# Performance work log

Measured on AMD Instinct MI355X. Metric: run time of the kernel, lower is better.

## Reference

```python
import jax, jax.numpy as jnp
import numpy as np

EMBED_DIM = 1024
N_HEADS = 16
HEAD_SIZE = EMBED_DIM // N_HEADS
SCALE = HEAD_SIZE ** -0.5


def setup_inputs() -> dict:
    key = jax.random.key(0)
    ks = jax.random.split(key, 11)
    B, Tq, Tk, C = 4, 1024, 1024, EMBED_DIM
    std = 0.02
    return {
        "q": jax.random.normal(ks[0], (B, Tq, C), jnp.float32),
        "k": jax.random.normal(ks[1], (B, Tk, C), jnp.float32),
        "v": jax.random.normal(ks[2], (B, Tk, C), jnp.float32),
        "Wq": jax.random.normal(ks[3], (C, C), jnp.float32) * std,
        "bq": jnp.zeros((C,), jnp.float32),
        "Wk": jax.random.normal(ks[4], (C, C), jnp.float32) * std,
        "bk": jnp.zeros((C,), jnp.float32),
        "Wv": jax.random.normal(ks[5], (C, C), jnp.float32) * std,
        "bv": jnp.zeros((C,), jnp.float32),
        "Wo": jax.random.normal(ks[6], (C, C), jnp.float32) * std,
        "bo": jnp.zeros((C,), jnp.float32),
    }


def reference(q, k, v, Wq, bq, Wk, bk, Wv, bv, Wo, bo):
    b, t, c = q.shape
    # linear projections (torch Linear: x @ W.T + b)
    qp = q @ Wq.T + bq            # [b, tq, c]
    kp = k @ Wk.T + bk            # [b, tk, c]
    vp = v @ Wv.T + bv            # [b, tk, c]
    # split heads: [b, h, t, d]
    qh = qp.reshape(b, t, N_HEADS, HEAD_SIZE).transpose(0, 2, 1, 3)
    kh = kp.reshape(b, kp.shape[1], N_HEADS, HEAD_SIZE).transpose(0, 2, 1, 3)
    vh = vp.reshape(b, vp.shape[1], N_HEADS, HEAD_SIZE).transpose(0, 2, 1, 3)
    # scaled dot-product attention
    scores = jnp.einsum('bhqd,bhkd->bhqk', qh, kh) * SCALE
    weights = jax.nn.softmax(scores, axis=-1)
    attn = jnp.einsum('bhqk,bhkd->bhqd', weights, vh)
    attn = attn.transpose(0, 2, 1, 3).reshape(b, t, c)
    out = attn @ Wo.T + bo
    return out
```

## Files before the change

kernel.cpp:

```cpp
#include <hip/hip_runtime.h>
#include <stdint.h>

typedef unsigned short u16;
typedef unsigned int   u32;
typedef __bf16 bf16;
typedef bf16  bf16x8 __attribute__((ext_vector_type(8)));
typedef float f32x4  __attribute__((ext_vector_type(4)));

#define AS1 __attribute__((address_space(1)))
#define AS3 __attribute__((address_space(3)))


__device__ __forceinline__ u16 f2bf(float f) {
  u32 u = __float_as_uint(f);
  return (u16)((u + 0x7fffu + ((u >> 16) & 1u)) >> 16);
}

__device__ __forceinline__ void gload_lds16(const void* src, void* dst) {
  __builtin_amdgcn_global_load_lds((const AS1 void*)src, (AS3 void*)dst, 16, 0, 0);
}

__device__ __forceinline__ bf16x8 fragL(const char* lds, int row, int kbyte) {
  return *(const bf16x8*)(lds + row * 128 + kbyte);
}


__global__ __launch_bounds__(256) void cvt_all(
    const float* q, const float* k, const float* v,
    const float* wq, const float* wk, const float* wv, const float* wo,
    u16* qb, u16* kb, u16* vb,
    u16* wqb, u16* wkb, u16* wvb, u16* wob)
{
  const float* src; u16* dst; int n4;
  switch (blockIdx.y) {
    case 0: src = q;  dst = qb;  n4 = 1048576; break;
    case 1: src = k;  dst = kb;  n4 = 1048576; break;
    case 2: src = v;  dst = vb;  n4 = 1048576; break;
    case 3: src = wq; dst = wqb; n4 = 262144;  break;
    case 4: src = wk; dst = wkb; n4 = 262144;  break;
    case 5: src = wv; dst = wvb; n4 = 262144;  break;
    default: src = wo; dst = wob; n4 = 262144; break;
  }
  int stride = gridDim.x * blockDim.x;
  for (int i = blockIdx.x * blockDim.x + threadIdx.x; i < n4; i += stride) {
    float4 f = ((const float4*)src)[i];
    ushort4 o;
    o.x = f2bf(f.x); o.y = f2bf(f.y); o.z = f2bf(f.z); o.w = f2bf(f.w);
    ((ushort4*)dst)[i] = o;
  }
}


__device__ __forceinline__ void stageL(const u16* gtile, char* lds, int tid)
{
  int w = tid >> 6, lane = tid & 63;
  int rr = lane >> 3;
  int cb = (lane & 7) << 4;
  #pragma unroll
  for (int i = 0; i < 4; ++i) {
    int c = i * 4 + w;
    gload_lds16((const char*)(gtile + (c * 8 + rr) * 1024) + cb, lds + c * 1024);
  }
}

__device__ __forceinline__ void gemm_core(const u16* A, const u16* W,
                                          f32x4 acc[4][4], int bi, int bj,
                                          int tid, char* As, char* Bs)
{
  int lane = tid & 63;
  int wr = (tid >> 7) & 1, wc = (tid >> 6) & 1;
  for (int kt = 0; kt < 16; ++kt) {
    stageL(A + bi * 128 * 1024 + kt * 64, As, tid);
    stageL(W + bj * 128 * 1024 + kt * 64, Bs, tid);
    __syncthreads();
    #pragma unroll
    for (int ks = 0; ks < 2; ++ks) {
      int kb = ks * 64 + ((lane >> 4) << 4);
      bf16x8 af[4], bfr[4];
      #pragma unroll
      for (int m = 0; m < 4; ++m) af[m]  = fragL(As, wr * 64 + m * 16 + (lane & 15), kb);
      #pragma unroll
      for (int n = 0; n < 4; ++n) bfr[n] = fragL(Bs, wc * 64 + n * 16 + (lane & 15), kb);
      #pragma unroll
      for (int m = 0; m < 4; ++m)
        #pragma unroll
        for (int n = 0; n < 4; ++n)
          acc[m][n] = __builtin_amdgcn_mfma_f32_16x16x32_bf16(af[m], bfr[n], acc[m][n], 0, 0, 0);
    }
    __syncthreads();
  }
}


__global__ __launch_bounds__(256, 2) void proj_gemm(
    const u16* qb, const u16* kb, const u16* vb,
    const u16* wqb, const u16* wkb, const u16* wvb,
    const float* bq, const float* bk, const float* bv,
    u16* qh, u16* kh, u16* vt)
{
  __shared__ alignas(16) char As[16384];
  __shared__ alignas(16) char Bs[16384];
  int tid = threadIdx.x;
  int bi = blockIdx.x & 31, bj = blockIdx.x >> 5;
  int z = blockIdx.z;
  const u16* A = (z == 0) ? qb : (z == 1) ? kb : vb;
  const u16* W = (z == 0) ? wqb : (z == 1) ? wkb : wvb;
  const float* bias = (z == 0) ? bq : (z == 1) ? bk : bv;
  u16* dst = (z == 0) ? qh : (z == 1) ? kh : vt;

  f32x4 acc[4][4] = {};
  gemm_core(A, W, acc, bi, bj, tid, As, Bs);

  int lane = tid & 63, wr = (tid >> 7) & 1, wc = (tid >> 6) & 1;
  int rbase = bi * 128 + wr * 64 + ((lane >> 4) << 2);
  int cbase = bj * 128 + wc * 64;
  #pragma unroll
  for (int n = 0; n < 4; ++n) {
    int col = cbase + n * 16 + (lane & 15);
    float bsv = bias[col];
    int h = col >> 6, d = col & 63;
    #pragma unroll
    for (int m = 0; m < 4; ++m) {
      #pragma unroll
      for (int r = 0; r < 4; ++r) {
        int R = rbase + m * 16 + r;
        int b = R >> 10, t = R & 1023;
        u16 val = f2bf(acc[m][n][r] + bsv);
        if (z < 2) dst[(((b * 16 + h) * 1024 + t) << 6) + d] = val;
        else       dst[(((b * 16 + h) * 64 + d) << 10) + t] = val;
      }
    }
  }
}


__global__ __launch_bounds__(256, 2) void out_gemm(
    const u16* attn, const u16* wob, const float* bo, float* out)
{
  __shared__ alignas(16) char As[16384];
  __shared__ alignas(16) char Bs[16384];
  int tid = threadIdx.x;
  int bi = blockIdx.x & 31, bj = blockIdx.x >> 5;

  f32x4 acc[4][4] = {};
  gemm_core(attn, wob, acc, bi, bj, tid, As, Bs);

  int lane = tid & 63, wr = (tid >> 7) & 1, wc = (tid >> 6) & 1;
  int rbase = bi * 128 + wr * 64 + ((lane >> 4) << 2);
  int cbase = bj * 128 + wc * 64;
  #pragma unroll
  for (int n = 0; n < 4; ++n) {
    int col = cbase + n * 16 + (lane & 15);
    float bsv = bo[col];
    #pragma unroll
    for (int m = 0; m < 4; ++m) {
      #pragma unroll
      for (int r = 0; r < 4; ++r) {
        int R = rbase + m * 16 + r;
        out[R * 1024 + col] = acc[m][n][r] + bsv;
      }
    }
  }
}


__global__ __launch_bounds__(256, 2) void attn_fwd(
    const u16* qh, const u16* kh, const u16* vt, u16* attnb)
{
  __shared__ alignas(16) u16 Ks[64 * 72];
  __shared__ alignas(16) u16 Vs[64 * 72];
  __shared__ alignas(16) u16 Pl[4][16 * 72];

  int tid = threadIdx.x, lane = tid & 63, w = tid >> 6;
  int g = lane >> 4;
  int q0 = blockIdx.x << 6;
  int bh = blockIdx.y;
  const u16* qbase = qh + bh * 65536;
  const u16* kbase = kh + bh * 65536;
  const u16* vbase = vt + bh * 65536;

  bf16x8 qf[2];
  {
    int qrow = q0 + w * 16 + (lane & 15);
    const u16* p = qbase + qrow * 64 + (g << 3);
    qf[0] = *(const bf16x8*)p;
    qf[1] = *(const bf16x8*)(p + 32);
  }

  f32x4 ot[4] = {};
  float m_r = -3.0e38f, l_r = 0.f;

  int sr = tid >> 2;
  int sj = (tid & 3) << 4;
  u16* pw = Pl[w];
  int prow = (lane & 15) * 72;

  for (int kv0 = 0; kv0 < 1024; kv0 += 64) {
    {
      const u16* ksrc = kbase + (kv0 + sr) * 64 + sj;
      const u16* vsrc = vbase + sr * 1024 + kv0 + sj;
      *(bf16x8*)(Ks + sr * 72 + sj)     = *(const bf16x8*)ksrc;
      *(bf16x8*)(Ks + sr * 72 + sj + 8) = *(const bf16x8*)(ksrc + 8);
      *(bf16x8*)(Vs + sr * 72 + sj)     = *(const bf16x8*)vsrc;
      *(bf16x8*)(Vs + sr * 72 + sj + 8) = *(const bf16x8*)(vsrc + 8);
    }
    __syncthreads();

    f32x4 sc[4] = {};
    #pragma unroll
    for (int ks = 0; ks < 2; ++ks) {
      #pragma unroll
      for (int m = 0; m < 4; ++m) {
        bf16x8 kf = *(const bf16x8*)(Ks + (m * 16 + (lane & 15)) * 72 + ks * 32 + g * 8);
        sc[m] = __builtin_amdgcn_mfma_f32_16x16x32_bf16(kf, qf[ks], sc[m], 0, 0, 0);
      }
    }

    float sv[4][4];
    float vmax = -3.0e38f;
    #pragma unroll
    for (int m = 0; m < 4; ++m)
      #pragma unroll
      for (int r = 0; r < 4; ++r) {
        sv[m][r] = sc[m][r] * 0.125f;
        vmax = fmaxf(vmax, sv[m][r]);
      }
    vmax = fmaxf(vmax, __shfl_xor(vmax, 16, 64));
    vmax = fmaxf(vmax, __shfl_xor(vmax, 32, 64));
    float mnew = fmaxf(m_r, vmax);
    float fac = __expf(m_r - mnew);
    float psum = 0.f;
    u32 pp[4][2];
    #pragma unroll
    for (int m = 0; m < 4; ++m) {
      float p0 = __expf(sv[m][0] - mnew);
      float p1 = __expf(sv[m][1] - mnew);
      float p2 = __expf(sv[m][2] - mnew);
      float p3 = __expf(sv[m][3] - mnew);
      psum += (p0 + p1) + (p2 + p3);
      pp[m][0] = (u32)f2bf(p0) | ((u32)f2bf(p1) << 16);
      pp[m][1] = (u32)f2bf(p2) | ((u32)f2bf(p3) << 16);
    }
    psum += __shfl_xor(psum, 16, 64);
    psum += __shfl_xor(psum, 32, 64);
    l_r = l_r * fac + psum;
    m_r = mnew;
    #pragma unroll
    for (int dm = 0; dm < 4; ++dm) ot[dm] *= fac;

    #pragma unroll
    for (int m = 0; m < 4; ++m) {
      u32* d = (u32*)(pw + prow + m * 16 + (g << 2));
      d[0] = pp[m][0];
      d[1] = pp[m][1];
    }

    #pragma unroll
    for (int ks = 0; ks < 2; ++ks) {
      bf16x8 pf = *(const bf16x8*)(pw + prow + ks * 32 + g * 8);
      #pragma unroll
      for (int dm = 0; dm < 4; ++dm) {
        bf16x8 vf = *(const bf16x8*)(Vs + (dm * 16 + (lane & 15)) * 72 + ks * 32 + g * 8);
        ot[dm] = __builtin_amdgcn_mfma_f32_16x16x32_bf16(vf, pf, ot[dm], 0, 0, 0);
      }
    }
    __syncthreads();
  }

  float inv = 1.0f / l_r;
  int b = bh >> 4, h = bh & 15;
  int tok = (b << 10) + q0 + w * 16 + (lane & 15);
  u16* obase = attnb + tok * 1024 + h * 64;
  #pragma unroll
  for (int dm = 0; dm < 4; ++dm) {
    int d0 = dm * 16 + (g << 2);
    u32 lo = (u32)f2bf(ot[dm][0] * inv) | ((u32)f2bf(ot[dm][1] * inv) << 16);
    u32 hi = (u32)f2bf(ot[dm][2] * inv) | ((u32)f2bf(ot[dm][3] * inv) << 16);
    u32* d = (u32*)(obase + d0);
    d[0] = lo; d[1] = hi;
  }
}


extern "C" void kernel_launch(void* const* d_in, const int* in_sizes, int n_in,
                              void* d_out, int out_size, void* d_ws, size_t ws_size,
                              hipStream_t stream)
{
  const float* q  = (const float*)d_in[0];
  const float* k  = (const float*)d_in[1];
  const float* v  = (const float*)d_in[2];
  const float* Wq = (const float*)d_in[3];
  const float* bq = (const float*)d_in[4];
  const float* Wk = (const float*)d_in[5];
  const float* bk = (const float*)d_in[6];
  const float* Wv = (const float*)d_in[7];
  const float* bv = (const float*)d_in[8];
  const float* Wo = (const float*)d_in[9];
  const float* bo = (const float*)d_in[10];
  float* out = (float*)d_out;

  u16* ws  = (u16*)d_ws;
  u16* qb  = ws;
  u16* kb  = qb  + (4u << 20);
  u16* vb  = kb  + (4u << 20);
  u16* wqb = vb  + (4u << 20);
  u16* wkb = wqb + (1u << 20);
  u16* wvb = wkb + (1u << 20);
  u16* wob = wvb + (1u << 20);
  u16* qhb = wob + (1u << 20);
  u16* khb = qhb + (4u << 20);
  u16* vtb = khb + (4u << 20);
  u16* atb = vtb + (4u << 20);

  cvt_all<<<dim3(1024, 7, 1), 256, 0, stream>>>(q, k, v, Wq, Wk, Wv, Wo,
                                                qb, kb, vb, wqb, wkb, wvb, wob);
  proj_gemm<<<dim3(256, 1, 3), 256, 0, stream>>>(qb, kb, vb, wqb, wkb, wvb,
                                                 bq, bk, bv, qhb, khb, vtb);
  attn_fwd<<<dim3(16, 64, 1), 256, 0, stream>>>(qhb, khb, vtb, atb);
  out_gemm<<<dim3(256, 1, 1), 256, 0, stream>>>(atb, wob, bo, out);
}
```

Measured before the change: 224.7 us.

## Load GEMM fragments directly to registers, prefetch KV, lazy softmax rescale, native bf16 cvt

The projection and output GEMMs drop LDS staging and barriers, and each wave loads its A and W MFMA fragments straight from global memory into registers. Without shared reuse, every wave re-reads its tiles from global or cache. The attention kernel prefetches the next K/V tile into registers while the current one is computed, folds the 0.125 scale into an fmaf, and skips the online-softmax rescale unless the running max grows past a threshold. Manual bf16 rounding is replaced by native bf16 conversions.

New measurement: 285.6 us. +27.1%, slower.

```diff
diff --git a/kernel.cpp b/kernel.cpp
--- a/kernel.cpp
+++ b/kernel.cpp
@@ -4,24 +4,21 @@
 typedef unsigned short u16;
 typedef unsigned int   u32;
 typedef __bf16 bf16;
+typedef bf16  bf16x2 __attribute__((ext_vector_type(2)));
 typedef bf16  bf16x8 __attribute__((ext_vector_type(8)));
 typedef float f32x4  __attribute__((ext_vector_type(4)));
 
-#define AS1 __attribute__((address_space(1)))
-#define AS3 __attribute__((address_space(3)))
-
-
-__device__ __forceinline__ u16 f2bf(float f) {
-  u32 u = __float_as_uint(f);
-  return (u16)((u + 0x7fffu + ((u >> 16) & 1u)) >> 16);
-}
-
-__device__ __forceinline__ void gload_lds16(const void* src, void* dst) {
-  __builtin_amdgcn_global_load_lds((const AS1 void*)src, (AS3 void*)dst, 16, 0, 0);
-}
-
-__device__ __forceinline__ bf16x8 fragL(const char* lds, int row, int kbyte) {
-  return *(const bf16x8*)(lds + row * 128 + kbyte);
+
+__device__ __forceinline__ u32 pk2(float lo, float hi) {
+  bf16x2 t;
+  t[0] = (bf16)lo;
+  t[1] = (bf16)hi;
+  return __builtin_bit_cast(u32, t);
+}
+
+__device__ __forceinline__ u16 b1(float f) {
+  bf16 t = (bf16)f;
+  return __builtin_bit_cast(u16, t);
 }
 
 
@@ -44,63 +41,48 @@
   int stride = gridDim.x * blockDim.x;
   for (int i = blockIdx.x * blockDim.x + threadIdx.x; i < n4; i += stride) {
     float4 f = ((const float4*)src)[i];
-    ushort4 o;
-    o.x = f2bf(f.x); o.y = f2bf(f.y); o.z = f2bf(f.z); o.w = f2bf(f.w);
-    ((ushort4*)dst)[i] = o;
-  }
-}
-
-
-__device__ __forceinline__ void stageL(const u16* gtile, char* lds, int tid)
-{
-  int w = tid >> 6, lane = tid & 63;
-  int rr = lane >> 3;
-  int cb = (lane & 7) << 4;
-  #pragma unroll
-  for (int i = 0; i < 4; ++i) {
-    int c = i * 4 + w;
-    gload_lds16((const char*)(gtile + (c * 8 + rr) * 1024) + cb, lds + c * 1024);
-  }
-}
-
-__device__ __forceinline__ void gemm_core(const u16* A, const u16* W,
-                                          f32x4 acc[4][4], int bi, int bj,
-                                          int tid, char* As, char* Bs)
-{
-  int lane = tid & 63;
-  int wr = (tid >> 7) & 1, wc = (tid >> 6) & 1;
+    uint2 o;
+    o.x = pk2(f.x, f.y);
+    o.y = pk2(f.z, f.w);
+    ((uint2*)dst)[i] = o;
+  }
+}
+
+
+__device__ __forceinline__ void gemm_core_reg(
+    const u16* Abase, const u16* Wbase, f32x4 acc[4][4])
+{
   for (int kt = 0; kt < 16; ++kt) {
-    stageL(A + bi * 128 * 1024 + kt * 64, As, tid);
-    stageL(W + bj * 128 * 1024 + kt * 64, Bs, tid);
-    __syncthreads();
-    #pragma unroll
-    for (int ks = 0; ks < 2; ++ks) {
-      int kb = ks * 64 + ((lane >> 4) << 4);
-      bf16x8 af[4], bfr[4];
-      #pragma unroll
-      for (int m = 0; m < 4; ++m) af[m]  = fragL(As, wr * 64 + m * 16 + (lane & 15), kb);
-      #pragma unroll
-      for (int n = 0; n < 4; ++n) bfr[n] = fragL(Bs, wc * 64 + n * 16 + (lane & 15), kb);
+    int ko = kt * 64;
+    bf16x8 af[4][2], bw[4][2];
+    #pragma unroll
+    for (int m = 0; m < 4; ++m) {
+      #pragma unroll
+      for (int ks = 0; ks < 2; ++ks) {
+        af[m][ks] = *(const bf16x8*)(Abase + m * 16384 + ko + ks * 32);
+        bw[m][ks] = *(const bf16x8*)(Wbase + m * 16384 + ko + ks * 32);
+      }
+    }
+    #pragma unroll
+    for (int ks = 0; ks < 2; ++ks)
       #pragma unroll
       for (int m = 0; m < 4; ++m)
         #pragma unroll
         for (int n = 0; n < 4; ++n)
-          acc[m][n] = __builtin_amdgcn_mfma_f32_16x16x32_bf16(af[m], bfr[n], acc[m][n], 0, 0, 0);
-    }
-    __syncthreads();
-  }
-}
-
-
-__global__ __launch_bounds__(256, 2) void proj_gemm(
+          acc[m][n] = __builtin_amdgcn_mfma_f32_16x16x32_bf16(
+              af[m][ks], bw[n][ks], acc[m][n], 0, 0, 0);
+  }
+}
+
+
+__global__ __launch_bounds__(256) void proj_gemm(
     const u16* qb, const u16* kb, const u16* vb,
     const u16* wqb, const u16* wkb, const u16* wvb,
     const float* bq, const float* bk, const float* bv,
     u16* qh, u16* kh, u16* vt)
 {
-  __shared__ alignas(16) char As[16384];
-  __shared__ alignas(16) char Bs[16384];
-  int tid = threadIdx.x;
+  int tid = threadIdx.x, lane = tid & 63;
+  int g = lane >> 4, r16 = lane & 15;
   int bi = blockIdx.x & 31, bj = blockIdx.x >> 5;
   int z = blockIdx.z;
   const u16* A = (z == 0) ? qb : (z == 1) ? kb : vb;
@@ -108,15 +90,18 @@
   const float* bias = (z == 0) ? bq : (z == 1) ? bk : bv;
   u16* dst = (z == 0) ? qh : (z == 1) ? kh : vt;
 
+  int wr = (tid >> 7) & 1, wc = (tid >> 6) & 1;
+  const u16* Abase = A + (bi * 128 + wr * 64 + r16) * 1024 + g * 8;
+  const u16* Wbase = W + (bj * 128 + wc * 64 + r16) * 1024 + g * 8;
+
   f32x4 acc[4][4] = {};
-  gemm_core(A, W, acc, bi, bj, tid, As, Bs);
-
-  int lane = tid & 63, wr = (tid >> 7) & 1, wc = (tid >> 6) & 1;
-  int rbase = bi * 128 + wr * 64 + ((lane >> 4) << 2);
+  gemm_core_reg(Abase, Wbase, acc);
+
+  int rbase = bi * 128 + wr * 64 + (g << 2);
   int cbase = bj * 128 + wc * 64;
   #pragma unroll
   for (int n = 0; n < 4; ++n) {
-    int col = cbase + n * 16 + (lane & 15);
+    int col = cbase + n * 16 + r16;
     float bsv = bias[col];
     int h = col >> 6, d = col & 63;
     #pragma unroll
@@ -125,7 +110,7 @@
       for (int r = 0; r < 4; ++r) {
         int R = rbase + m * 16 + r;
         int b = R >> 10, t = R & 1023;
-        u16 val = f2bf(acc[m][n][r] + bsv);
+        u16 val = b1(acc[m][n][r] + bsv);
         if (z < 2) dst[(((b * 16 + h) * 1024 + t) << 6) + d] = val;
         else       dst[(((b * 16 + h) * 64 + d) << 10) + t] = val;
       }
@@ -134,23 +119,25 @@
 }
 
 
-__global__ __launch_bounds__(256, 2) void out_gemm(
+__global__ __launch_bounds__(256) void out_gemm(
     const u16* attn, const u16* wob, const float* bo, float* out)
 {
-  __shared__ alignas(16) char As[16384];
-  __shared__ alignas(16) char Bs[16384];
-  int tid = threadIdx.x;
+  int tid = threadIdx.x, lane = tid & 63;
+  int g = lane >> 4, r16 = lane & 15;
   int bi = blockIdx.x & 31, bj = blockIdx.x >> 5;
 
+  int wr = (tid >> 7) & 1, wc = (tid >> 6) & 1;
+  const u16* Abase = attn + (bi * 128 + wr * 64 + r16) * 1024 + g * 8;
+  const u16* Wbase = wob + (bj * 128 + wc * 64 + r16) * 1024 + g * 8;
+
   f32x4 acc[4][4] = {};
-  gemm_core(attn, wob, acc, bi, bj, tid, As, Bs);
-
-  int lane = tid & 63, wr = (tid >> 7) & 1, wc = (tid >> 6) & 1;
-  int rbase = bi * 128 + wr * 64 + ((lane >> 4) << 2);
+  gemm_core_reg(Abase, Wbase, acc);
+
+  int rbase = bi * 128 + wr * 64 + (g << 2);
   int cbase = bj * 128 + wc * 64;
   #pragma unroll
   for (int n = 0; n < 4; ++n) {
-    int col = cbase + n * 16 + (lane & 15);
+    int col = cbase + n * 16 + r16;
     float bsv = bo[col];
     #pragma unroll
     for (int m = 0; m < 4; ++m) {
@@ -170,6 +157,9 @@
   __shared__ alignas(16) u16 Ks[64 * 72];
   __shared__ alignas(16) u16 Vs[64 * 72];
   __shared__ alignas(16) u16 Pl[4][16 * 72];
+
+  const float SC = 0.125f;
+  const float RTHR = 64.0f;
 
   int tid = threadIdx.x, lane = tid & 63, w = tid >> 6;
   int g = lane >> 4;
@@ -195,16 +185,30 @@
   u16* pw = Pl[w];
   int prow = (lane & 15) * 72;
 
+  const u16* ksrc0 = kbase + sr * 64 + sj;
+  const u16* vsrc0 = vbase + sr * 1024 + sj;
+
+  bf16x8 kr0, kr1, vr0, vr1;
+  kr0 = *(const bf16x8*)(ksrc0);
+  kr1 = *(const bf16x8*)(ksrc0 + 8);
+  vr0 = *(const bf16x8*)(vsrc0);
+  vr1 = *(const bf16x8*)(vsrc0 + 8);
+
   for (int kv0 = 0; kv0 < 1024; kv0 += 64) {
-    {
-      const u16* ksrc = kbase + (kv0 + sr) * 64 + sj;
-      const u16* vsrc = vbase + sr * 1024 + kv0 + sj;
-      *(bf16x8*)(Ks + sr * 72 + sj)     = *(const bf16x8*)ksrc;
-      *(bf16x8*)(Ks + sr * 72 + sj + 8) = *(const bf16x8*)(ksrc + 8);
-      *(bf16x8*)(Vs + sr * 72 + sj)     = *(const bf16x8*)vsrc;
-      *(bf16x8*)(Vs + sr * 72 + sj + 8) = *(const bf16x8*)(vsrc + 8);
-    }
+    *(bf16x8*)(Ks + sr * 72 + sj)     = kr0;
+    *(bf16x8*)(Ks + sr * 72 + sj + 8) = kr1;
+    *(bf16x8*)(Vs + sr * 72 + sj)     = vr0;
+    *(bf16x8*)(Vs + sr * 72 + sj + 8) = vr1;
     __syncthreads();
+
+    if (kv0 < 960) {
+      const u16* kn = ksrc0 + (kv0 + 64) * 64;
+      const u16* vn = vsrc0 + (kv0 + 64);
+      kr0 = *(const bf16x8*)(kn);
+      kr1 = *(const bf16x8*)(kn + 8);
+      vr0 = *(const bf16x8*)(vn);
+      vr1 = *(const bf16x8*)(vn + 8);
+    }
 
     f32x4 sc[4] = {};
     #pragma unroll
@@ -216,37 +220,40 @@
       }
     }
 
-    float sv[4][4];
     float vmax = -3.0e38f;
     #pragma unroll
     for (int m = 0; m < 4; ++m)
       #pragma unroll
-      for (int r = 0; r < 4; ++r) {
-        sv[m][r] = sc[m][r] * 0.125f;
-        vmax = fmaxf(vmax, sv[m][r]);
-      }
+      for (int r = 0; r < 4; ++r)
+        vmax = fmaxf(vmax, sc[m][r]);
     vmax = fmaxf(vmax, __shfl_xor(vmax, 16, 64));
     vmax = fmaxf(vmax, __shfl_xor(vmax, 32, 64));
-    float mnew = fmaxf(m_r, vmax);
-    float fac = __expf(m_r - mnew);
+
+    if (!__all(vmax - m_r <= RTHR)) {
+      float mnew = fmaxf(m_r, vmax);
+      float fac = __expf((m_r - mnew) * SC);
+      l_r *= fac;
+      #pragma unroll
+      for (int dm = 0; dm < 4; ++dm) ot[dm] *= fac;
+      m_r = mnew;
+    }
+    float nm = -m_r * SC;
+
     float psum = 0.f;
     u32 pp[4][2];
     #pragma unroll
     for (int m = 0; m < 4; ++m) {
-      float p0 = __expf(sv[m][0] - mnew);
-      float p1 = __expf(sv[m][1] - mnew);
-      float p2 = __expf(sv[m][2] - mnew);
-      float p3 = __expf(sv[m][3] - mnew);
+      float p0 = __expf(fmaf(sc[m][0], SC, nm));
+      float p1 = __expf(fmaf(sc[m][1], SC, nm));
+      float p2 = __expf(fmaf(sc[m][2], SC, nm));
+      float p3 = __expf(fmaf(sc[m][3], SC, nm));
       psum += (p0 + p1) + (p2 + p3);
-      pp[m][0] = (u32)f2bf(p0) | ((u32)f2bf(p1) << 16);
-      pp[m][1] = (u32)f2bf(p2) | ((u32)f2bf(p3) << 16);
+      pp[m][0] = pk2(p0, p1);
+      pp[m][1] = pk2(p2, p3);
     }
     psum += __shfl_xor(psum, 16, 64);
     psum += __shfl_xor(psum, 32, 64);
-    l_r = l_r * fac + psum;
-    m_r = mnew;
-    #pragma unroll
-    for (int dm = 0; dm < 4; ++dm) ot[dm] *= fac;
+    l_r += psum;
 
     #pragma unroll
     for (int m = 0; m < 4; ++m) {
@@ -274,10 +281,9 @@
   #pragma unroll
   for (int dm = 0; dm < 4; ++dm) {
     int d0 = dm * 16 + (g << 2);
-    u32 lo = (u32)f2bf(ot[dm][0] * inv) | ((u32)f2bf(ot[dm][1] * inv) << 16);
-    u32 hi = (u32)f2bf(ot[dm][2] * inv) | ((u32)f2bf(ot[dm][3] * inv) << 16);
     u32* d = (u32*)(obase + d0);
-    d[0] = lo; d[1] = hi;
+    d[0] = pk2(ot[dm][0] * inv, ot[dm][1] * inv);
+    d[1] = pk2(ot[dm][2] * inv, ot[dm][3] * inv);
   }
 }
 
```
